# Kernel optimization log

Hardware: AMD Instinct MI355X
Metric: run time of the kernel (lower is better)

Reference implementation:

```python
import jax, jax.numpy as jnp
import numpy as np


def _mind_pairs():
    # Replicates Mind3D.__init__ shift-pair construction (static, numpy).
    P = np.array([[0, 1, 1], [1, 1, 0], [1, 0, 1], [1, 1, 2], [2, 1, 1], [1, 2, 1]])
    d2 = ((P[:, None, :] - P[None, :, :]) ** 2).sum(-1)
    i, j = np.meshgrid(np.arange(6), np.arange(6), indexing='ij')
    mask = (i > j) & (d2 == 2)
    return P[i[mask]], P[j[mask]]  # each (12, 3), entries in {0,1,2}


_IDX1, _IDX2 = _mind_pairs()
_DILATION = 2
_RADIUS = 2


def setup_inputs() -> dict:
    key = jax.random.key(0)
    x = jax.random.uniform(key, (2, 1, 128, 128, 128), dtype=jnp.float32)
    return {"x": x}


def _shift(xp, idx, out_shape):
    # xp: [B,1,D+6,H+6,W+6]; one-hot 3x3x3 kernel at idx with dilation 2 and
    # conv zero-pad 1 is equivalent to a slice starting at 2*idx.
    i, j, k = (2 * int(idx[0]), 2 * int(idx[1]), 2 * int(idx[2]))
    D, H, W = out_shape
    return xp[:, 0, i:i + D, j:j + H, k:k + W]


def reference(x):
    d, r = _DILATION, _RADIUS
    # Normalize (empty-stats path): min/max over whole tensor
    vmin = x.min()
    x = (x - vmin) / (x.max() - vmin + 1e-6)

    B, _, D, H, W = x.shape
    out_sp = (D + 2, H + 2, W + 2)  # conv output spatial size
    # replication pad by dilation, then zero pad by 1 (conv padding=1)
    xp = jnp.pad(x, ((0, 0), (0, 0), (d, d), (d, d), (d, d)), mode='edge')
    xp = jnp.pad(xp, ((0, 0), (0, 0), (1, 1), (1, 1), (1, 1)))

    # 12 shift-pair squared differences -> [B,12,D+2,H+2,W+2]
    diff_sq = jnp.stack(
        [(_shift(xp, _IDX1[c], out_sp) - _shift(xp, _IDX2[c], out_sp)) ** 2
         for c in range(12)], axis=1)

    # replication pad by radius, then 5^3 avg pool stride 1 (VALID)
    sp = jnp.pad(diff_sq, ((0, 0), (0, 0), (r, r), (r, r), (r, r)), mode='edge')
    k = 2 * r + 1
    ssd = jax.lax.reduce_window(sp, 0.0, jax.lax.add,
                                (1, 1, k, k, k), (1, 1, 1, 1, 1), 'VALID')
    ssd = ssd / float(k ** 3)

    mind = ssd - ssd.min(axis=1, keepdims=True)
    mind_var = mind.mean(axis=1, keepdims=True)
    m = mind_var.mean()
    mind_var = jnp.clip(mind_var, m * 0.001, m * 1000.0)
    mind = jnp.exp(-mind / mind_var)
    return mind
```

## Files before the change

kernel.cpp:

```cpp
#include <hip/hip_runtime.h>

#define V 2197000
#define NV4 549250
#define VPL 16900
#define DQY 17
#define DQZ 14
#define NROWS 238
#define A4P 20
#define A4SZ (NROWS*A4P)
#define NXY 90
#define NWG 2340

__device__ __forceinline__ void load_row(const float* __restrict__ g, int ax0, int klass,
                                         bool zero, float (&r)[24]){
  if (zero){
    #pragma unroll
    for (int j=0;j<24;++j) r[j]=0.f;
    return;
  }
  const float4* p = (const float4*)(g + ax0);
  if (klass==1){
    float vv[28];
    #pragma unroll
    for (int j=0;j<7;++j){ float4 v=p[j]; vv[4*j]=v.x; vv[4*j+1]=v.y; vv[4*j+2]=v.z; vv[4*j+3]=v.w; }
    #pragma unroll
    for (int j=0;j<24;++j) r[j]=vv[j+3];
  } else if (klass==0){
    float vv[24];
    #pragma unroll
    for (int j=0;j<6;++j){ float4 v=p[j]; vv[4*j]=v.x; vv[4*j+1]=v.y; vv[4*j+2]=v.z; vv[4*j+3]=v.w; }
    r[0]=0.f; r[1]=vv[0]; r[2]=vv[0]; r[3]=vv[0];
    #pragma unroll
    for (int j=4;j<24;++j) r[j]=vv[j-3];
  } else if (klass==2){
    float vv[24];
    #pragma unroll
    for (int j=0;j<6;++j){ float4 v=p[j]; vv[4*j]=v.x; vv[4*j+1]=v.y; vv[4*j+2]=v.z; vv[4*j+3]=v.w; }
    #pragma unroll
    for (int j=0;j<21;++j) r[j]=vv[j+3];
    r[21]=vv[23]; r[22]=vv[23]; r[23]=0.f;
  } else {
    float4 v0=p[0], v1=p[1];
    r[0]=v0.w; r[1]=v1.x; r[2]=v1.y; r[3]=v1.z; r[4]=v1.w;
    r[5]=v1.w; r[6]=v1.w;
    #pragma unroll
    for (int j=7;j<24;++j) r[j]=0.f;
  }
}

template<int S1X, int S2X>
__device__ __forceinline__ void aphase(const float (&r1)[24], const float (&r2)[24],
                                       float* __restrict__ buf, const int (&wb)[4],
                                       int bxg, bool arow){
  if (!arow) return;
  float dd[20];
  #pragma unroll
  for (int t=0;t<20;++t){ float d = r1[t+S1X]-r2[t+S2X]; dd[t]=d*d; }
  float W[16];
  W[0]=dd[0]+dd[1]+dd[2]+dd[3]+dd[4];
  #pragma unroll
  for (int j=1;j<16;++j) W[j]=W[j-1]+dd[j+4]-dd[j-1];
  float Ao[16];
  if (bxg==0){
    Ao[0]=W[0]+2.f*dd[0]-dd[3]-dd[4];
    Ao[1]=W[0]+dd[0]-dd[4];
    #pragma unroll
    for(int j=2;j<16;++j) Ao[j]=W[j-2];
  } else if (bxg==8){
    Ao[0]=W[0]+dd[3]-dd[4];
    Ao[1]=W[0]-dd[0]+2.f*dd[3]-dd[4];
    #pragma unroll
    for(int j=2;j<16;++j) Ao[j]=W[j-2];
  } else {
    #pragma unroll
    for(int j=0;j<16;++j) Ao[j]=W[j];
  }
  #pragma unroll
  for (int q=0;q<4;++q)
    *(float4*)(buf + wb[q]) = make_float4(Ao[4*q],Ao[4*q+1],Ao[4*q+2],Ao[4*q+3]);
}

__device__ __forceinline__ void yzphase(const float* __restrict__ buf, const int (&yb)[5],
                                        bool yzact, bool valid, float* __restrict__ gp,
                                        float (&rmin)[10], float (&rsum)[10],
                                        bool first, int cV){
  if (!yzact) return;
  float By[14];
  #pragma unroll
  for (int z=0;z<14;++z){
    By[z] = buf[yb[0]+z*A4P] + buf[yb[1]+z*A4P] + buf[yb[2]+z*A4P]
          + buf[yb[3]+z*A4P] + buf[yb[4]+z*A4P];
  }
  float S = By[0]+By[1]+By[2]+By[3]+By[4];
  #pragma unroll
  for (int k=0;k<10;++k){
    if (valid) gp[cV + k*VPL] = S;
    if (first){ rmin[k]=S; rsum[k]=S; }
    else      { rmin[k]=fminf(rmin[k],S); rsum[k]+=S; }
    if (k<9) S += By[k+5]-By[k];
  }
}

#define PIN24(r) asm volatile("" : \
  "+v"(r[0]),"+v"(r[1]),"+v"(r[2]),"+v"(r[3]),"+v"(r[4]),"+v"(r[5]), \
  "+v"(r[6]),"+v"(r[7]),"+v"(r[8]),"+v"(r[9]),"+v"(r[10]),"+v"(r[11]), \
  "+v"(r[12]),"+v"(r[13]),"+v"(r[14]),"+v"(r[15]),"+v"(r[16]),"+v"(r[17]), \
  "+v"(r[18]),"+v"(r[19]),"+v"(r[20]),"+v"(r[21]),"+v"(r[22]),"+v"(r[23]))

__global__ __launch_bounds__(256,3) void mind_main(const float* __restrict__ x,
                                                   float* __restrict__ pre,
                                                   float* __restrict__ bsum){
  __shared__ float A4[2*A4SZ];
  __shared__ float wred[4];

  const int tid = threadIdx.x;
  const int orig = blockIdx.x;
  const int xcd = orig & 7, posi = orig >> 3;
  const int t = (xcd < 4) ? xcd*293 + posi : 1172 + (xcd-4)*292 + posi;
  const int xyb = t % NXY;
  const int rest = t / NXY;
  const int zb = rest % 13;
  const int b  = rest / 13;
  const int bxg = xyb % 9, byg = xyb / 9;
  const int p0x = bxg*16, p0y = byg*13, p0z = zb*10;

  const float* xb = x + b*2097152;
  const int ax0   = (bxg==0) ? 0 : 16*bxg-8;
  const int klass = (bxg==0) ? 0 : (bxg<=6) ? 1 : (bxg==7) ? 2 : 3;

  const bool arow = tid < NROWS;
  const int tz = tid/DQY, ty = tid - tz*DQY;
  const int ez = min(max(p0z-2+tz,0),129);
  const int ey = min(max(p0y-2+ty,0),129);
  const int izA = min(max(ez-1,0),127);
  const int izC = min(ez+1,127);
  const int izE = max(ez-3,0);
  const int iyA = min(max(ey-1,0),127);
  const int iyB = max(ey-3,0);
  const int iyD = min(ey+1,127);
  const bool zB = (ey==0), zD = (ey==129), zE = (ez==0), zC = (ez==129);
  const float* gA = xb + (izA*128+iyA)*128;
  const float* gB = xb + (izA*128+iyB)*128;
  const float* gC = xb + (izC*128+iyA)*128;
  const float* gD = xb + (izA*128+iyD)*128;
  const float* gE = xb + (izE*128+iyA)*128;

  int wb[4];
  {
    const int wrow = ty*DQZ + tz;
    #pragma unroll
    for (int q=0;q<4;++q) wb[q] = wrow*A4P + ((q+ty)%5)*4;
  }

  const int oyT = tid>>4, oxT = tid&15;
  const bool yzact = tid < 208;
  const bool valid = yzact && (p0x + oxT < 130);
  int yb[5];
  {
    const int ox2 = oxT>>2, oxe = oxT&3;
    #pragma unroll
    for (int y5=0;y5<5;++y5){
      const int yy = oyT + y5;
      yb[y5] = yy*(DQZ*A4P) + ((ox2 + yy)%5)*4 + oxe;
    }
  }
  float* gp = pre + ((long)b*12*V + p0z*VPL + (p0y+oyT)*130 + (p0x+oxT));
  float rmin[10], rsum[10];

  float* const b0 = A4;
  float* const b1 = A4 + A4SZ;

  float rA[24],rB[24],rC[24],rD[24],rE[24];
  if (arow){
    load_row(gB,ax0,klass,zB,rB);
    load_row(gE,ax0,klass,zE,rE);
    load_row(gA,ax0,klass,false,rA);
    load_row(gD,ax0,klass,zD,rD);
    PIN24(rB); PIN24(rE); PIN24(rA); PIN24(rD);
  }

  aphase<2,2>(rB,rE,b0,wb,bxg,arow);
  __syncthreads();
  aphase<0,2>(rA,rE,b1,wb,bxg,arow);
  yzphase(b0,yb,yzact,valid,gp,rmin,rsum,true , 1*V);
  __syncthreads();
  aphase<4,2>(rA,rE,b0,wb,bxg,arow);
  yzphase(b1,yb,yzact,valid,gp,rmin,rsum,false, 0*V);
  __syncthreads();
  aphase<2,2>(rD,rE,b1,wb,bxg,arow);
  if (arow){ load_row(gC,ax0,klass,zC,rC); PIN24(rC); }
  yzphase(b0,yb,yzact,valid,gp,rmin,rsum,false, 3*V);
  __syncthreads();
  aphase<2,0>(rB,rA,b0,wb,bxg,arow);
  yzphase(b1,yb,yzact,valid,gp,rmin,rsum,false, 8*V);
  __syncthreads();
  aphase<4,2>(rA,rB,b1,wb,bxg,arow);
  yzphase(b0,yb,yzact,valid,gp,rmin,rsum,false, 2*V);
  __syncthreads();
  aphase<2,2>(rC,rB,b0,wb,bxg,arow);
  yzphase(b1,yb,yzact,valid,gp,rmin,rsum,false, 4*V);
  __syncthreads();
  aphase<2,0>(rC,rA,b1,wb,bxg,arow);
  yzphase(b0,yb,yzact,valid,gp,rmin,rsum,false, 6*V);
  __syncthreads();
  aphase<2,4>(rC,rA,b0,wb,bxg,arow);
  yzphase(b1,yb,yzact,valid,gp,rmin,rsum,false, 5*V);
  __syncthreads();
  aphase<2,2>(rD,rC,b1,wb,bxg,arow);
  yzphase(b0,yb,yzact,valid,gp,rmin,rsum,false, 7*V);
  __syncthreads();
  aphase<2,0>(rD,rA,b0,wb,bxg,arow);
  yzphase(b1,yb,yzact,valid,gp,rmin,rsum,false,11*V);
  __syncthreads();
  aphase<2,4>(rD,rA,b1,wb,bxg,arow);
  yzphase(b0,yb,yzact,valid,gp,rmin,rsum,false, 9*V);
  __syncthreads();
  yzphase(b1,yb,yzact,valid,gp,rmin,rsum,false,10*V);

  float vl = 0.f;
  if (valid){
    #pragma unroll
    for (int k=0;k<10;++k) vl += rsum[k]*(1.0f/12.0f) - rmin[k];
  }
  #pragma unroll
  for (int off=32; off>0; off>>=1) vl += __shfl_down(vl, off, 64);
  if ((tid&63)==0) wred[tid>>6] = vl;
  __syncthreads();
  if (tid==0) bsum[orig] = wred[0]+wred[1]+wred[2]+wred[3];
}

__global__ __launch_bounds__(256) void reduce_bsum(const float* __restrict__ bsum, float* wsf){
  __shared__ float sm[256];
  float s = 0.f;
  for (int i = threadIdx.x; i < NWG; i += 256) s += bsum[i];
  sm[threadIdx.x] = s;
  __syncthreads();
  for (int w = 128; w > 0; w >>= 1){
    if (threadIdx.x < w) sm[threadIdx.x] += sm[threadIdx.x + w];
    __syncthreads();
  }
  if (threadIdx.x == 0) wsf[2] = sm[0] * (1.0f/4394000.0f);
}

__global__ __launch_bounds__(256) void final_kernel(float* __restrict__ out,
                                                    const float* __restrict__ wsf){
  const int q = blockIdx.x*256 + threadIdx.x;
  if (q >= 2*NV4) return;
  const float m = wsf[2];
  const float lo = m*0.001f, hi = m*1000.f;
  const int b = q / NV4;
  const int vq = q - b*NV4;
  float4* o4 = (float4*)out;
  const int ob = b*12*NV4 + vq;
  float4 p[12];
  #pragma unroll
  for (int c=0;c<12;++c) p[c] = o4[ob + c*NV4];
  float4 mn = p[0], sm = p[0];
  #pragma unroll
  for (int c=1;c<12;++c){
    mn.x = fminf(mn.x,p[c].x); mn.y = fminf(mn.y,p[c].y);
    mn.z = fminf(mn.z,p[c].z); mn.w = fminf(mn.w,p[c].w);
    sm.x += p[c].x; sm.y += p[c].y; sm.z += p[c].z; sm.w += p[c].w;
  }
  const float rx = 1.f/fminf(fmaxf(sm.x*(1.f/12.f)-mn.x, lo), hi);
  const float ry = 1.f/fminf(fmaxf(sm.y*(1.f/12.f)-mn.y, lo), hi);
  const float rz = 1.f/fminf(fmaxf(sm.z*(1.f/12.f)-mn.z, lo), hi);
  const float rw = 1.f/fminf(fmaxf(sm.w*(1.f/12.f)-mn.w, lo), hi);
  #pragma unroll
  for (int c=0;c<12;++c){
    float4 e;
    e.x = __expf(-(p[c].x-mn.x)*rx);
    e.y = __expf(-(p[c].y-mn.y)*ry);
    e.z = __expf(-(p[c].z-mn.z)*rz);
    e.w = __expf(-(p[c].w-mn.w)*rw);
    o4[ob + c*NV4] = e;
  }
}

extern "C" void kernel_launch(void* const* d_in, const int* in_sizes, int n_in,
                              void* d_out, int out_size, void* d_ws, size_t ws_size,
                              hipStream_t stream){
  (void)in_sizes; (void)n_in; (void)out_size; (void)ws_size;
  const float* x = (const float*)d_in[0];
  float* out = (float*)d_out;
  float* wsf = (float*)d_ws;
  float* bsum = (float*)((char*)d_ws + 64);

  hipLaunchKernelGGL(mind_main, dim3(NWG), dim3(256), 0, stream, x, out, bsum);
  hipLaunchKernelGGL(reduce_bsum, dim3(1), dim3(256), 0, stream, bsum, wsf);
  hipLaunchKernelGGL(final_kernel, dim3((2*NV4+255)/256), dim3(256), 0, stream, out, wsf);
}
```

Baseline: 178.4 us.

## Enlarge z-tile to 11 outputs and reorganize shared-memory staging layout

Increases the per-block z output depth from 10 to 11 (12 z-blocks instead of 13), so 255 of 256 threads stage rows and fewer blocks recompute halo. The shared-memory layout is reorganized with z-major row indexing, a 24-float padded stride, and a 6-way rotated bank swizzle. Bounds checks are added for the partial last z-block. The shared buffer grows, which may reduce occupancy, and the last z-block wastes some work.

```diff
diff --git a/kernel.cpp b/kernel.cpp
--- a/kernel.cpp
+++ b/kernel.cpp
@@ -3,13 +3,15 @@
 #define V 2197000
 #define NV4 549250
 #define VPL 16900
+#define TZ 11
 #define DQY 17
-#define DQZ 14
-#define NROWS 238
-#define A4P 20
+#define DQZ 15
+#define NROWS 255
+#define A4P 24
 #define A4SZ (NROWS*A4P)
 #define NXY 90
-#define NWG 2340
+#define NZB 12
+#define NWG 2160
 
 __device__ __forceinline__ void load_row(const float* __restrict__ g, int ax0, int klass,
                                          bool zero, float (&r)[24]){
@@ -80,24 +82,25 @@
     *(float4*)(buf + wb[q]) = make_float4(Ao[4*q],Ao[4*q+1],Ao[4*q+2],Ao[4*q+3]);
 }
 
-__device__ __forceinline__ void yzphase(const float* __restrict__ buf, const int (&yb)[5],
-                                        bool yzact, bool valid, float* __restrict__ gp,
-                                        float (&rmin)[10], float (&rsum)[10],
+__device__ __forceinline__ void yzphase(const float* __restrict__ buf, const int (&bset)[6],
+                                        bool yzact, bool valid, int p0z,
+                                        float* __restrict__ gp,
+                                        float (&rmin)[TZ], float (&rsum)[TZ],
                                         bool first, int cV){
   if (!yzact) return;
-  float By[14];
-  #pragma unroll
-  for (int z=0;z<14;++z){
-    By[z] = buf[yb[0]+z*A4P] + buf[yb[1]+z*A4P] + buf[yb[2]+z*A4P]
-          + buf[yb[3]+z*A4P] + buf[yb[4]+z*A4P];
+  float By[15];
+  #pragma unroll
+  for (int z=0;z<15;++z){
+    const int bo = bset[z%6] + z*A4P;
+    By[z] = buf[bo] + buf[bo+360] + buf[bo+720] + buf[bo+1080] + buf[bo+1440];
   }
   float S = By[0]+By[1]+By[2]+By[3]+By[4];
   #pragma unroll
-  for (int k=0;k<10;++k){
-    if (valid) gp[cV + k*VPL] = S;
+  for (int k=0;k<TZ;++k){
+    if (valid && (p0z + k) < 130) gp[cV + k*VPL] = S;
     if (first){ rmin[k]=S; rsum[k]=S; }
     else      { rmin[k]=fminf(rmin[k],S); rsum[k]+=S; }
-    if (k<9) S += By[k+5]-By[k];
+    if (k<TZ-1) S += By[k+5]-By[k];
   }
 }
 
@@ -116,22 +119,22 @@
   const int tid = threadIdx.x;
   const int orig = blockIdx.x;
   const int xcd = orig & 7, posi = orig >> 3;
-  const int t = (xcd < 4) ? xcd*293 + posi : 1172 + (xcd-4)*292 + posi;
+  const int t = xcd*270 + posi;
   const int xyb = t % NXY;
   const int rest = t / NXY;
-  const int zb = rest % 13;
-  const int b  = rest / 13;
+  const int zb = rest % NZB;
+  const int b  = rest / NZB;
   const int bxg = xyb % 9, byg = xyb / 9;
-  const int p0x = bxg*16, p0y = byg*13, p0z = zb*10;
+  const int p0x = bxg*16, p0y = byg*13, p0z = zb*TZ;
 
   const float* xb = x + b*2097152;
   const int ax0   = (bxg==0) ? 0 : 16*bxg-8;
   const int klass = (bxg==0) ? 0 : (bxg<=6) ? 1 : (bxg==7) ? 2 : 3;
 
   const bool arow = tid < NROWS;
-  const int tz = tid/DQY, ty = tid - tz*DQY;
-  const int ez = min(max(p0z-2+tz,0),129);
-  const int ey = min(max(p0y-2+ty,0),129);
+  const int yA = tid/DQZ, zA = tid - yA*DQZ;
+  const int ez = min(max(p0z-2+zA,0),129);
+  const int ey = min(max(p0y-2+yA,0),129);
   const int izA = min(max(ez-1,0),127);
   const int izC = min(ez+1,127);
   const int izE = max(ez-3,0);
@@ -147,25 +150,28 @@
 
   int wb[4];
   {
-    const int wrow = ty*DQZ + tz;
-    #pragma unroll
-    for (int q=0;q<4;++q) wb[q] = wrow*A4P + ((q+ty)%5)*4;
+    const int zm = zA%6;
+    #pragma unroll
+    for (int q=0;q<4;++q){
+      int s = q + zm; if (s>=6) s-=6;
+      wb[q] = tid*A4P + s*4;
+    }
   }
 
   const int oyT = tid>>4, oxT = tid&15;
   const bool yzact = tid < 208;
   const bool valid = yzact && (p0x + oxT < 130);
-  int yb[5];
+  int bset[6];
   {
     const int ox2 = oxT>>2, oxe = oxT&3;
     #pragma unroll
-    for (int y5=0;y5<5;++y5){
-      const int yy = oyT + y5;
-      yb[y5] = yy*(DQZ*A4P) + ((ox2 + yy)%5)*4 + oxe;
+    for (int j=0;j<6;++j){
+      int s = ox2 + j; if (s>=6) s-=6;
+      bset[j] = oyT*360 + s*4 + oxe;
     }
   }
   float* gp = pre + ((long)b*12*V + p0z*VPL + (p0y+oyT)*130 + (p0x+oxT));
-  float rmin[10], rsum[10];
+  float rmin[TZ], rsum[TZ];
 
   float* const b0 = A4;
   float* const b1 = A4 + A4SZ;
@@ -182,45 +188,46 @@
   aphase<2,2>(rB,rE,b0,wb,bxg,arow);
   __syncthreads();
   aphase<0,2>(rA,rE,b1,wb,bxg,arow);
-  yzphase(b0,yb,yzact,valid,gp,rmin,rsum,true , 1*V);
+  yzphase(b0,bset,yzact,valid,p0z,gp,rmin,rsum,true , 1*V);
   __syncthreads();
   aphase<4,2>(rA,rE,b0,wb,bxg,arow);
-  yzphase(b1,yb,yzact,valid,gp,rmin,rsum,false, 0*V);
+  yzphase(b1,bset,yzact,valid,p0z,gp,rmin,rsum,false, 0*V);
   __syncthreads();
   aphase<2,2>(rD,rE,b1,wb,bxg,arow);
   if (arow){ load_row(gC,ax0,klass,zC,rC); PIN24(rC); }
-  yzphase(b0,yb,yzact,valid,gp,rmin,rsum,false, 3*V);
+  yzphase(b0,bset,yzact,valid,p0z,gp,rmin,rsum,false, 3*V);
   __syncthreads();
   aphase<2,0>(rB,rA,b0,wb,bxg,arow);
-  yzphase(b1,yb,yzact,valid,gp,rmin,rsum,false, 8*V);
+  yzphase(b1,bset,yzact,valid,p0z,gp,rmin,rsum,false, 8*V);
   __syncthreads();
   aphase<4,2>(rA,rB,b1,wb,bxg,arow);
-  yzphase(b0,yb,yzact,valid,gp,rmin,rsum,false, 2*V);
+  yzphase(b0,bset,yzact,valid,p0z,gp,rmin,rsum,false, 2*V);
   __syncthreads();
   aphase<2,2>(rC,rB,b0,wb,bxg,arow);
-  yzphase(b1,yb,yzact,valid,gp,rmin,rsum,false, 4*V);
+  yzphase(b1,bset,yzact,valid,p0z,gp,rmin,rsum,false, 4*V);
   __syncthreads();
   aphase<2,0>(rC,rA,b1,wb,bxg,arow);
-  yzphase(b0,yb,yzact,valid,gp,rmin,rsum,false, 6*V);
+  yzphase(b0,bset,yzact,valid,p0z,gp,rmin,rsum,false, 6*V);
   __syncthreads();
   aphase<2,4>(rC,rA,b0,wb,bxg,arow);
-  yzphase(b1,yb,yzact,valid,gp,rmin,rsum,false, 5*V);
+  yzphase(b1,bset,yzact,valid,p0z,gp,rmin,rsum,false, 5*V);
   __syncthreads();
   aphase<2,2>(rD,rC,b1,wb,bxg,arow);
-  yzphase(b0,yb,yzact,valid,gp,rmin,rsum,false, 7*V);
+  yzphase(b0,bset,yzact,valid,p0z,gp,rmin,rsum,false, 7*V);
   __syncthreads();
   aphase<2,0>(rD,rA,b0,wb,bxg,arow);
-  yzphase(b1,yb,yzact,valid,gp,rmin,rsum,false,11*V);
+  yzphase(b1,bset,yzact,valid,p0z,gp,rmin,rsum,false,11*V);
   __syncthreads();
   aphase<2,4>(rD,rA,b1,wb,bxg,arow);
-  yzphase(b0,yb,yzact,valid,gp,rmin,rsum,false, 9*V);
-  __syncthreads();
-  yzphase(b1,yb,yzact,valid,gp,rmin,rsum,false,10*V);
+  yzphase(b0,bset,yzact,valid,p0z,gp,rmin,rsum,false, 9*V);
+  __syncthreads();
+  yzphase(b1,bset,yzact,valid,p0z,gp,rmin,rsum,false,10*V);
 
   float vl = 0.f;
   if (valid){
     #pragma unroll
-    for (int k=0;k<10;++k) vl += rsum[k]*(1.0f/12.0f) - rmin[k];
+    for (int k=0;k<TZ;++k)
+      if (p0z + k < 130) vl += rsum[k]*(1.0f/12.0f) - rmin[k];
   }
   #pragma unroll
   for (int off=32; off>0; off>>=1) vl += __shfl_down(vl, off, 64);
```

After: 235.7 us. 1.32x slower.

## Rework LDS layout and yz-phase thread mapping to process float2 pairs

Applied to the files above, without the earlier changes.

Shrinks the LDS row pitch from 20 to 16 floats and changes the write swizzle to a 4-way rotation. Each yz-phase thread now handles two adjacent x outputs as float2 over half the z range (5 outputs instead of 10), with 9 box-sum rows instead of 14. Output stores become float2 wide. Occupancy hint rises from 3 to 4 blocks per CU. This aims to cut LDS footprint and per-thread register use and to widen LDS reads and global stores, at the risk of new bank conflicts and of an incorrect index mapping.

```diff
diff --git a/kernel.cpp b/kernel.cpp
--- a/kernel.cpp
+++ b/kernel.cpp
@@ -3,12 +3,14 @@
 #define V 2197000
 #define NV4 549250
 #define VPL 16900
+#define TZ 10
 #define DQY 17
 #define DQZ 14
 #define NROWS 238
-#define A4P 20
+#define A4P 16
 #define A4SZ (NROWS*A4P)
 #define NXY 90
+#define NZB 13
 #define NWG 2340
 
 __device__ __forceinline__ void load_row(const float* __restrict__ g, int ax0, int klass,
@@ -80,24 +82,34 @@
     *(float4*)(buf + wb[q]) = make_float4(Ao[4*q],Ao[4*q+1],Ao[4*q+2],Ao[4*q+3]);
 }
 
-__device__ __forceinline__ void yzphase(const float* __restrict__ buf, const int (&yb)[5],
+__device__ __forceinline__ void yzphase(const float2* __restrict__ a2, const int (&fb)[5],
                                         bool yzact, bool valid, float* __restrict__ gp,
-                                        float (&rmin)[10], float (&rsum)[10],
+                                        float2 (&rmin)[5], float2 (&rsum)[5],
                                         bool first, int cV){
   if (!yzact) return;
-  float By[14];
-  #pragma unroll
-  for (int z=0;z<14;++z){
-    By[z] = buf[yb[0]+z*A4P] + buf[yb[1]+z*A4P] + buf[yb[2]+z*A4P]
-          + buf[yb[3]+z*A4P] + buf[yb[4]+z*A4P];
-  }
-  float S = By[0]+By[1]+By[2]+By[3]+By[4];
-  #pragma unroll
-  for (int k=0;k<10;++k){
-    if (valid) gp[cV + k*VPL] = S;
-    if (first){ rmin[k]=S; rsum[k]=S; }
-    else      { rmin[k]=fminf(rmin[k],S); rsum[k]+=S; }
-    if (k<9) S += By[k+5]-By[k];
+  float2 By[9];
+  #pragma unroll
+  for (int zl=0; zl<9; ++zl){
+    float2 a0 = a2[fb[0] + zl*136];
+    float2 a1 = a2[fb[1] + zl*136];
+    float2 a3 = a2[fb[2] + zl*136];
+    float2 a4 = a2[fb[3] + zl*136];
+    float2 a5 = a2[fb[4] + zl*136];
+    By[zl].x = a0.x+a1.x+a3.x+a4.x+a5.x;
+    By[zl].y = a0.y+a1.y+a3.y+a4.y+a5.y;
+  }
+  float2 S;
+  S.x = By[0].x+By[1].x+By[2].x+By[3].x+By[4].x;
+  S.y = By[0].y+By[1].y+By[2].y+By[3].y+By[4].y;
+  #pragma unroll
+  for (int j=0;j<5;++j){
+    if (valid) *(float2*)(gp + cV + j*VPL) = S;
+    if (first){ rmin[j]=S; rsum[j]=S; }
+    else {
+      rmin[j].x = fminf(rmin[j].x,S.x); rmin[j].y = fminf(rmin[j].y,S.y);
+      rsum[j].x += S.x;                 rsum[j].y += S.y;
+    }
+    if (j<4){ S.x += By[j+5].x-By[j].x; S.y += By[j+5].y-By[j].y; }
   }
 }
 
@@ -107,7 +119,7 @@
   "+v"(r[12]),"+v"(r[13]),"+v"(r[14]),"+v"(r[15]),"+v"(r[16]),"+v"(r[17]), \
   "+v"(r[18]),"+v"(r[19]),"+v"(r[20]),"+v"(r[21]),"+v"(r[22]),"+v"(r[23]))
 
-__global__ __launch_bounds__(256,3) void mind_main(const float* __restrict__ x,
+__global__ __launch_bounds__(256,4) void mind_main(const float* __restrict__ x,
                                                    float* __restrict__ pre,
                                                    float* __restrict__ bsum){
   __shared__ float A4[2*A4SZ];
@@ -119,10 +131,10 @@
   const int t = (xcd < 4) ? xcd*293 + posi : 1172 + (xcd-4)*292 + posi;
   const int xyb = t % NXY;
   const int rest = t / NXY;
-  const int zb = rest % 13;
-  const int b  = rest / 13;
+  const int zb = rest % NZB;
+  const int b  = rest / NZB;
   const int bxg = xyb % 9, byg = xyb / 9;
-  const int p0x = bxg*16, p0y = byg*13, p0z = zb*10;
+  const int p0x = bxg*16, p0y = byg*13, p0z = zb*TZ;
 
   const float* xb = x + b*2097152;
   const int ax0   = (bxg==0) ? 0 : 16*bxg-8;
@@ -146,27 +158,24 @@
   const float* gE = xb + (izE*128+iyA)*128;
 
   int wb[4];
-  {
-    const int wrow = ty*DQZ + tz;
-    #pragma unroll
-    for (int q=0;q<4;++q) wb[q] = wrow*A4P + ((q+ty)%5)*4;
-  }
-
-  const int oyT = tid>>4, oxT = tid&15;
+  #pragma unroll
+  for (int q=0;q<4;++q) wb[q] = tid*A4P + ((q+ty)&3)*4;
+
+  const int oy = tid>>4, xh = (tid>>1)&7, zh = tid&1;
+  const int xq = xh>>1, jo = xh&1;
   const bool yzact = tid < 208;
-  const bool valid = yzact && (p0x + oxT < 130);
-  int yb[5];
-  {
-    const int ox2 = oxT>>2, oxe = oxT&3;
-    #pragma unroll
-    for (int y5=0;y5<5;++y5){
-      const int yy = oyT + y5;
-      yb[y5] = yy*(DQZ*A4P) + ((ox2 + yy)%5)*4 + oxe;
-    }
-  }
-  float* gp = pre + ((long)b*12*V + p0z*VPL + (p0y+oyT)*130 + (p0x+oxT));
-  float rmin[10], rsum[10];
-
+  const bool valid = yzact && ((bxg<8) || (xh==0));
+  int fb[5];
+  #pragma unroll
+  for (int y5=0;y5<5;++y5){
+    const int row0 = 85*zh + oy + y5;
+    fb[y5] = row0*8 + ((xq + oy + y5)&3)*2 + jo;
+  }
+  float* gp = pre + ((long)b*12*V + (p0z + 5*zh)*VPL + (p0y+oy)*130 + (p0x + 2*xh));
+  float2 rmin[5], rsum[5];
+
+  const float2* const a20 = (const float2*)A4;
+  const float2* const a21 = (const float2*)(A4 + A4SZ);
   float* const b0 = A4;
   float* const b1 = A4 + A4SZ;
 
@@ -182,45 +191,47 @@
   aphase<2,2>(rB,rE,b0,wb,bxg,arow);
   __syncthreads();
   aphase<0,2>(rA,rE,b1,wb,bxg,arow);
-  yzphase(b0,yb,yzact,valid,gp,rmin,rsum,true , 1*V);
+  yzphase(a20,fb,yzact,valid,gp,rmin,rsum,true , 1*V);
   __syncthreads();
   aphase<4,2>(rA,rE,b0,wb,bxg,arow);
-  yzphase(b1,yb,yzact,valid,gp,rmin,rsum,false, 0*V);
+  yzphase(a21,fb,yzact,valid,gp,rmin,rsum,false, 0*V);
   __syncthreads();
   aphase<2,2>(rD,rE,b1,wb,bxg,arow);
   if (arow){ load_row(gC,ax0,klass,zC,rC); PIN24(rC); }
-  yzphase(b0,yb,yzact,valid,gp,rmin,rsum,false, 3*V);
+  yzphase(a20,fb,yzact,valid,gp,rmin,rsum,false, 3*V);
   __syncthreads();
   aphase<2,0>(rB,rA,b0,wb,bxg,arow);
-  yzphase(b1,yb,yzact,valid,gp,rmin,rsum,false, 8*V);
+  yzphase(a21,fb,yzact,valid,gp,rmin,rsum,false, 8*V);
   __syncthreads();
   aphase<4,2>(rA,rB,b1,wb,bxg,arow);
-  yzphase(b0,yb,yzact,valid,gp,rmin,rsum,false, 2*V);
+  yzphase(a20,fb,yzact,valid,gp,rmin,rsum,false, 2*V);
   __syncthreads();
   aphase<2,2>(rC,rB,b0,wb,bxg,arow);
-  yzphase(b1,yb,yzact,valid,gp,rmin,rsum,false, 4*V);
+  yzphase(a21,fb,yzact,valid,gp,rmin,rsum,false, 4*V);
   __syncthreads();
   aphase<2,0>(rC,rA,b1,wb,bxg,arow);
-  yzphase(b0,yb,yzact,valid,gp,rmin,rsum,false, 6*V);
+  yzphase(a20,fb,yzact,valid,gp,rmin,rsum,false, 6*V);
   __syncthreads();
   aphase<2,4>(rC,rA,b0,wb,bxg,arow);
-  yzphase(b1,yb,yzact,valid,gp,rmin,rsum,false, 5*V);
+  yzphase(a21,fb,yzact,valid,gp,rmin,rsum,false, 5*V);
   __syncthreads();
   aphase<2,2>(rD,rC,b1,wb,bxg,arow);
-  yzphase(b0,yb,yzact,valid,gp,rmin,rsum,false, 7*V);
+  yzphase(a20,fb,yzact,valid,gp,rmin,rsum,false, 7*V);
   __syncthreads();
   aphase<2,0>(rD,rA,b0,wb,bxg,arow);
-  yzphase(b1,yb,yzact,valid,gp,rmin,rsum,false,11*V);
+  yzphase(a21,fb,yzact,valid,gp,rmin,rsum,false,11*V);
   __syncthreads();
   aphase<2,4>(rD,rA,b1,wb,bxg,arow);
-  yzphase(b0,yb,yzact,valid,gp,rmin,rsum,false, 9*V);
-  __syncthreads();
-  yzphase(b1,yb,yzact,valid,gp,rmin,rsum,false,10*V);
+  yzphase(a20,fb,yzact,valid,gp,rmin,rsum,false, 9*V);
+  __syncthreads();
+  yzphase(a21,fb,yzact,valid,gp,rmin,rsum,false,10*V);
 
   float vl = 0.f;
   if (valid){
     #pragma unroll
-    for (int k=0;k<10;++k) vl += rsum[k]*(1.0f/12.0f) - rmin[k];
+    for (int j=0;j<5;++j)
+      vl += (rsum[j].x*(1.0f/12.0f) - rmin[j].x)
+          + (rsum[j].y*(1.0f/12.0f) - rmin[j].y);
   }
   #pragma unroll
   for (int off=32; off>0; off>>=1) vl += __shfl_down(vl, off, 64);
```

New measurement: 539.9 us. +202.6%, slower.
